# Kernel tuning notes

Measured on AMD Instinct MI355X. Metric: run time of the kernel, lower is better.

## Reference

```python
import jax, jax.numpy as jnp
import numpy as np

EPS = 1e-6
INF = 1e30  # stands in for 'no value' in the sparse C_bar lists of the torch code


def setup_inputs() -> dict:
    key = jax.random.key(0)
    M, N, D = 512, 256, 64
    kx, ky, kq = jax.random.split(key, 3)
    x = jax.random.normal(kx, (M, D), dtype=jnp.float32)
    y = jax.random.normal(ky, (N, D), dtype=jnp.float32)
    u = jax.random.uniform(kq, (N + 1, N), dtype=jnp.float32, minval=0.05, maxval=1.0)
    q = u / jnp.sum(u, axis=0, keepdims=True)  # column-stochastic jump probabilities
    return {"x": x, "y": y, "q": q}


def _pal_forward(x, y, q):
    M, N = x.shape[0], y.shape[0]
    dt = x.dtype

    # ---- compute_dists: pairwise L2 (p=2 norm), M x N ----
    diff = x[:, None, :] - y[None, :, :]
    dists = jnp.sqrt(jnp.sum(diff * diff, axis=2))

    # ---- compute_reachability: sequential accumulation over columns of q ----
    def reach_step(p, nb):
        return p + p[nb] * q[:, nb], None
    p0 = jnp.zeros(N + 1, dtype=dt).at[0].set(1.0)
    p, _ = jax.lax.scan(reach_step, p0, jnp.arange(N))
    p_back = p[:N][None, :] * q / (p[:, None] + EPS)  # (N+1, N)

    # ---- edge structure: ancestors n_bar < n with p_back > 0 (detached mask) ----
    tri = jnp.tril(jnp.ones((N, N), dtype=bool), k=-1)
    E = tri & (jax.lax.stop_gradient(p_back[:N]) > 0)   # (N, N): E[n, n_bar]
    w = jnp.where(E, p_back[:N], 0.0)                   # mixing weights

    ns = jnp.arange(1, N)

    def row_dp(d_row, base0, C_prev, Cbar_prev):
        """One row m of the lattice. C_prev: C[m-1] (N,), Cbar_prev: C_bar[m-1] (N,N).
        Returns C[m] (N,) and C_bar[m] (N,N) with INF at non-edge slots."""
        C0 = jnp.zeros(N, dtype=dt).at[0].set(d_row[0] + base0)

        def n_step(Ccur, n):
            # min over: C[m][n_bar] (insert y), C[m-1][n_bar] (match), C_bar[m-1][n][n_bar] (insert x)
            c_min = jnp.minimum(Ccur, jnp.minimum(C_prev, Cbar_prev[n]))  # (N,) over n_bar
            cbar = d_row[n] + c_min
            val = jnp.sum(jnp.where(E[n], w[n] * cbar, 0.0))
            return Ccur.at[n].set(val), jnp.where(E[n], cbar, INF)

        C_row, Cbar_rows = jax.lax.scan(n_step, C0, ns)
        Cbar = jnp.concatenate([jnp.full((1, N), INF, dt), Cbar_rows], axis=0)
        return C_row, Cbar

    # m = 0: no previous row -> previous-row candidates disabled via INF, C[0][0] = d[0,0]
    C_row0, Cbar0 = row_dp(dists[0], jnp.zeros((), dt), jnp.full(N, INF, dt), jnp.full((N, N), INF, dt))

    def m_step(carry, d_row):
        C_prev, Cbar_prev = carry
        C_row, Cbar = row_dp(d_row, C_prev[0], C_prev, Cbar_prev)  # C[m][0] = d[m,0] + C[m-1][0]
        return (C_row, Cbar), None

    (C_last, _), _ = jax.lax.scan(m_step, (C_row0, Cbar0), dists[1:])

    # expected cost of reaching END from each terminal n
    return jnp.sum(p_back[N] * C_last)


def reference(x, y, q):
    return _pal_forward(x, y, q)
```

## Files before the change

kernel.cpp:

```cpp
#include <hip/hip_runtime.h>

typedef float f4 __attribute__((ext_vector_type(4)));

#define Nn 256
#define Mm 512
#define Dd 64
#define EPSF 1e-6f
#define INFF 1e30f
#define BC 8
#define NCHUNK (Nn / BC)
#define R 16
#define NBLK 8
#define WVS 4
#define SST (NBLK * WVS)
#define SLOTS 4

#define OFF_D     0
#define OFF_QC    131072
#define OFF_P     (OFF_QC + 65792)
#define OFF_WT    (OFF_P + 260)
#define OFF_WS    (OFF_WT + 65536)
#define OFF_CBAR  (OFF_WS + 256)
#define OFF_CROW  (OFF_CBAR + 65536)
#define OFF_FLAG  (OFF_CROW + SST*Nn)

__device__ __forceinline__ int llc_load_int(const int* p) {
  int v;
  asm volatile("global_load_dword %0, %1, off sc0 sc1\n\ts_waitcnt vmcnt(0)"
               : "=v"(v) : "v"(p) : "memory");
  return v;
}
__device__ __forceinline__ void llc_store_int(int* p, int v) {
  asm volatile("global_store_dword %0, %1, off sc0 sc1" :: "v"(p), "v"(v) : "memory");
}
__device__ __forceinline__ void llc_load_cbar10(const float* b0, const float* cp,
                                                f4 c[8], f4& pl, f4& ph) {
  const float* b1 = b0 + 4 * Nn;
  asm volatile(
    "global_load_dwordx4 %0, %10, off sc0 sc1\n\t"
    "global_load_dwordx4 %1, %10, off offset:1024 sc0 sc1\n\t"
    "global_load_dwordx4 %2, %10, off offset:2048 sc0 sc1\n\t"
    "global_load_dwordx4 %3, %10, off offset:3072 sc0 sc1\n\t"
    "global_load_dwordx4 %4, %11, off sc0 sc1\n\t"
    "global_load_dwordx4 %5, %11, off offset:1024 sc0 sc1\n\t"
    "global_load_dwordx4 %6, %11, off offset:2048 sc0 sc1\n\t"
    "global_load_dwordx4 %7, %11, off offset:3072 sc0 sc1\n\t"
    "global_load_dwordx4 %8, %12, off sc0 sc1\n\t"
    "global_load_dwordx4 %9, %12, off offset:16 sc0 sc1\n\t"
    "s_waitcnt vmcnt(0)"
    : "=v"(c[0]), "=v"(c[1]), "=v"(c[2]), "=v"(c[3]),
      "=v"(c[4]), "=v"(c[5]), "=v"(c[6]), "=v"(c[7]),
      "=v"(pl), "=v"(ph)
    : "v"(b0), "v"(b1), "v"(cp)
    : "memory");
}
__device__ __forceinline__ void llc_store_cbar8(float* b0, const f4 c[8]) {
  float* b1 = b0 + 4 * Nn;
  asm volatile(
    "global_store_dwordx4 %8, %0, off sc0 sc1\n\t"
    "global_store_dwordx4 %8, %1, off offset:1024 sc0 sc1\n\t"
    "global_store_dwordx4 %8, %2, off offset:2048 sc0 sc1\n\t"
    "global_store_dwordx4 %8, %3, off offset:3072 sc0 sc1\n\t"
    "global_store_dwordx4 %9, %4, off sc0 sc1\n\t"
    "global_store_dwordx4 %9, %5, off offset:1024 sc0 sc1\n\t"
    "global_store_dwordx4 %9, %6, off offset:2048 sc0 sc1\n\t"
    "global_store_dwordx4 %9, %7, off offset:3072 sc0 sc1\n\t"
    "s_waitcnt vmcnt(0)"
    :: "v"(c[0]), "v"(c[1]), "v"(c[2]), "v"(c[3]),
       "v"(c[4]), "v"(c[5]), "v"(c[6]), "v"(c[7]),
       "v"(b0), "v"(b1)
    : "memory");
}
__device__ __forceinline__ float rdlane(float v, int l) {
  return __int_as_float(__builtin_amdgcn_readlane(__float_as_int(v), l));
}

__global__ __launch_bounds__(256) void k_pre(const float* __restrict__ x,
                                             const float* __restrict__ y,
                                             const float* __restrict__ q,
                                             float* __restrict__ ws) {
  const int b = blockIdx.x, t = threadIdx.x;
  if (b < Mm) {
    __shared__ float xs[Dd];
    if (t < Dd) xs[t] = x[b * Dd + t];
    __syncthreads();
    const float4* y4 = (const float4*)(y + t * Dd);
    float acc = 0.f;
#pragma unroll
    for (int k = 0; k < Dd / 4; k++) {
      float4 v = y4[k];
      float a0 = xs[4*k+0] - v.x, a1 = xs[4*k+1] - v.y;
      float a2 = xs[4*k+2] - v.z, a3 = xs[4*k+3] - v.w;
      acc += a0*a0 + a1*a1 + a2*a2 + a3*a3;
    }
    ws[OFF_D + b * Nn + t] = sqrtf(acc);
  } else if (b < Mm + 257) {
    const int j = b - Mm;
    ws[OFF_QC + t * 257 + j] = q[j * Nn + t];
  } else {
    ((int*)(ws + OFF_FLAG))[t] = 0;
  }
}

__global__ __launch_bounds__(256) void k_reach(const float* __restrict__ q, float* __restrict__ p_out) {
  __shared__ float p[257];
  __shared__ float vsnap[64];
  __shared__ float qtile[64][65];
  int tid = threadIdx.x;
  p[tid] = (tid == 0) ? 1.f : 0.f;
  if (tid == 0) p[256] = 0.f;
  __syncthreads();
  for (int g = 0; g < 4; g++) {
    int g0 = g * 64;
    for (int z = 0; z < 16; z++) {
      int idx = tid + z * 256, l = idx >> 6, k = idx & 63;
      qtile[k][l] = q[(g0 + l) * Nn + g0 + k];
    }
    __syncthreads();
    if (tid < 64) {
      float pv = p[g0 + tid];
      for (int k = 0; k < 64; k++) {
        float v = __shfl(pv, k, 64);
        if (tid == k) vsnap[k] = v;
        pv += v * qtile[k][tid];
      }
    }
    __syncthreads();
    float4 qs[16];
    const float4* qrow = (const float4*)(q + tid * Nn + g0);
#pragma unroll
    for (int i = 0; i < 16; i++) qs[i] = qrow[i];
    float acc = p[tid];
#pragma unroll
    for (int i = 0; i < 16; i++) {
      acc += vsnap[4*i+0] * qs[i].x;
      acc += vsnap[4*i+1] * qs[i].y;
      acc += vsnap[4*i+2] * qs[i].z;
      acc += vsnap[4*i+3] * qs[i].w;
    }
    float acc2 = 0.f;
    if (tid == 0) {
      acc2 = p[256];
      const float4* qlast = (const float4*)(q + 256 * Nn + g0);
#pragma unroll
      for (int i = 0; i < 16; i++) {
        float4 v = qlast[i];
        acc2 += vsnap[4*i+0] * v.x + vsnap[4*i+1] * v.y
              + vsnap[4*i+2] * v.z + vsnap[4*i+3] * v.w;
      }
    }
    __syncthreads();
    p[tid] = acc;
    if (tid == 0) p[256] = acc2;
    __syncthreads();
  }
  p_out[tid] = p[tid];
  if (tid == 0) p_out[256] = p[256];
}

__global__ __launch_bounds__(256) void k_wbuild(const float* __restrict__ qc, const float* __restrict__ p,
                                                float* __restrict__ wT) {
  int t = blockIdx.x, n = threadIdx.x;
  float v = 0.f;
  if (t < n) v = p[t] * qc[t * 257 + n] / (p[n] + EPSF);
  wT[t * Nn + n] = v;
}

__global__ __launch_bounds__(256, 1) void k_main(const float* __restrict__ d,
                                                 const float* __restrict__ wT,
                                                 float* __restrict__ cbarG,
                                                 float* __restrict__ crowG,
                                                 int* __restrict__ flags,
                                                 const float* __restrict__ q,
                                                 const float* __restrict__ p,
                                                 float* __restrict__ out) {
  __shared__ __align__(16) float sbuf[SLOTS][BC * Nn];
  __shared__ __align__(16) float crow_lds[WVS][SLOTS][BC];
  __shared__ __align__(16) float crow_fin[Nn];

  const int tid  = threadIdx.x;
  const int wave = tid >> 6;
  const int lane = tid & 63;
  const int blk  = blockIdx.x;
  const int stage = blk * WVS + wave;
  const int m0 = stage * R;

  f4 dl[R], S[R];
#pragma unroll
  for (int r = 0; r < R; r++) {
    dl[r] = *(const f4*)(d + (m0 + r) * Nn + 4 * lane);
    S[r] = (f4){0.f, 0.f, 0.f, 0.f};
  }
  f4 Wt = (f4){0.f, 0.f, 0.f, 0.f};
#pragma unroll 8
  for (int t = 0; t < Nn; t++)
    Wt += *(const f4*)(wT + t * Nn + 4 * lane);

#pragma clang loop unroll(disable)
  for (int s = 0; s < NCHUNK + WVS - 1; s++) {
    const int j = s - wave;
    if (j >= 0 && j < NCHUNK) {
      f4 wv[BC];
#pragma unroll
      for (int tt = 0; tt < BC; tt++)
        wv[tt] = *(const f4*)(wT + (j * BC + tt) * Nn + 4 * lane);

      f4 c[BC], cpl, cph;
      float* lsl = &sbuf[j & (SLOTS - 1)][0] + 4 * lane;

      if (wave == 0) {
        if (blk > 0) {
          const int* fp = flags + (blk - 1) * NCHUNK + j;
          while (llc_load_int(fp) == 0) __builtin_amdgcn_s_sleep(1);
          llc_load_cbar10(cbarG + (size_t)j * BC * Nn + 4 * lane,
                          crowG + (blk - 1) * Nn + j * BC, c, cpl, cph);
        } else {
          cpl = (f4){INFF, INFF, INFF, INFF};
          cph = cpl;
#pragma unroll
          for (int tt = 0; tt < BC; tt++) c[tt] = cpl;
        }
      } else {
#pragma unroll
        for (int tt = 0; tt < BC; tt++) c[tt] = *(const f4*)(lsl + tt * Nn);
        const float* cr = &crow_lds[wave - 1][j & (SLOTS - 1)][0];
        cpl = *(const f4*)cr;
        cph = *(const f4*)(cr + 4);
      }

      f4 clast4;
      const bool isJ0 = (j == 0);
#pragma unroll
      for (int tt = 0; tt < BC; tt++) {
        const int owner = 2 * j + (tt >> 2);
        const int comp = tt & 3;
        const bool isT0 = isJ0 && (tt == 0);

        float up = (tt < 4) ? cpl[comp] : cph[comp];
        float prcMin = up;
        float prcVal = up;
        if (isT0 && stage == 0) prcVal = 0.f;
        float cml[R];
#pragma unroll
        for (int r = 0; r < R; r++) {
          float Cv;
          if (isT0) Cv = dl[r][0] + prcVal;
          else      Cv = fmaf(dl[r][comp], Wt[comp], S[r][comp]);
          cml[r] = fminf(Cv, prcMin);
          prcVal = Cv;
          prcMin = Cv;
        }
        float cmB[R];
#pragma unroll
        for (int r = 0; r < R; r++) cmB[r] = rdlane(cml[r], owner);
        float clastv = rdlane(prcVal, owner);
        if (lane == owner) clast4[comp] = clastv;

#pragma unroll
        for (int k = 0; k < 4; k++) {
          float w_ = wv[tt][k];
          if (w_ > 0.f) {
            float cbv = c[tt][k];
#pragma unroll
            for (int r = 0; r < R; r++) {
              float a = fminf(cmB[r], cbv);
              S[r][k] = fmaf(w_, a, S[r][k]);
              cbv = dl[r][k] + a;
            }
            c[tt][k] = cbv;
          }
        }
      }

      if (wave < WVS - 1) {
#pragma unroll
        for (int tt = 0; tt < BC; tt++) *(f4*)(lsl + tt * Nn) = c[tt];
        if (lane == 2 * j || lane == 2 * j + 1)
          *(f4*)&crow_lds[wave][j & (SLOTS - 1)][(lane & 1) * 4] = clast4;
      } else if (blk < NBLK - 1) {
        if (lane == 2 * j || lane == 2 * j + 1) {
          float* cp = crowG + blk * Nn + j * BC + (lane & 1) * 4;
          asm volatile("global_store_dwordx4 %0, %1, off sc0 sc1" :: "v"(cp), "v"(clast4) : "memory");
        }
        llc_store_cbar8(cbarG + (size_t)j * BC * Nn + 4 * lane, c);
        if (lane == 0) llc_store_int(flags + blk * NCHUNK + j, 1);
      } else {
        if (lane == 2 * j || lane == 2 * j + 1)
          *(f4*)&crow_fin[j * BC + (lane & 1) * 4] = clast4;
      }
    }
    __syncthreads();
  }

  if (blk == NBLK - 1) {
    float fw = p[tid] * q[Nn * Nn + tid] / (p[Nn] + EPSF);
    crow_fin[tid] *= fw;
    __syncthreads();
    for (int sft = 128; sft > 0; sft >>= 1) {
      if (tid < sft) crow_fin[tid] += crow_fin[tid + sft];
      __syncthreads();
    }
    if (tid == 0) out[0] = crow_fin[0];
  }
}

extern "C" void kernel_launch(void* const* d_in, const int* in_sizes, int n_in,
                              void* d_out, int out_size, void* d_ws, size_t ws_size,
                              hipStream_t stream) {
  const float* x = (const float*)d_in[0];
  const float* y = (const float*)d_in[1];
  const float* q = (const float*)d_in[2];
  float* ws = (float*)d_ws;
  float* out = (float*)d_out;
  hipLaunchKernelGGL(k_pre,   dim3(Mm + 257 + 1), dim3(256), 0, stream, x, y, q, ws);
  hipLaunchKernelGGL(k_reach, dim3(1),   dim3(256), 0, stream, q, ws + OFF_P);
  hipLaunchKernelGGL(k_wbuild,dim3(Nn),  dim3(256), 0, stream, ws + OFF_QC, ws + OFF_P,
                     ws + OFF_WT);
  hipLaunchKernelGGL(k_main,  dim3(NBLK), dim3(256), 0, stream, ws + OFF_D, ws + OFF_WT,
                     ws + OFF_CBAR, ws + OFF_CROW, (int*)(ws + OFF_FLAG),
                     q, ws + OFF_P, out);
}
```

Baseline: 466.7 us.

## Fuse reachability and weight-building kernels into the main wavefront kernel

Removes the separate single-block reachability kernel and the weight-matrix build kernel. Each main-kernel block now recomputes the reachability vector redundantly in shared memory and derives mixing weights on the fly from the transposed q and p, instead of reading a precomputed wT. The transposed q stride is padded to 260 so rows are 16-byte aligned for vector loads. This saves two launches and a global round trip, at the cost of every block repeating the serial reachability scan and doing extra arithmetic per chunk.

```diff
diff --git a/kernel.cpp b/kernel.cpp
--- a/kernel.cpp
+++ b/kernel.cpp
@@ -14,13 +14,11 @@
 #define WVS 4
 #define SST (NBLK * WVS)
 #define SLOTS 4
+#define QSTR 260
 
 #define OFF_D     0
 #define OFF_QC    131072
-#define OFF_P     (OFF_QC + 65792)
-#define OFF_WT    (OFF_P + 260)
-#define OFF_WS    (OFF_WT + 65536)
-#define OFF_CBAR  (OFF_WS + 256)
+#define OFF_CBAR  (OFF_QC + 67072)
 #define OFF_CROW  (OFF_CBAR + 65536)
 #define OFF_FLAG  (OFF_CROW + SST*Nn)
 
@@ -96,19 +94,35 @@
     ws[OFF_D + b * Nn + t] = sqrtf(acc);
   } else if (b < Mm + 257) {
     const int j = b - Mm;
-    ws[OFF_QC + t * 257 + j] = q[j * Nn + t];
+    ws[OFF_QC + t * QSTR + j] = q[j * Nn + t];
   } else {
     ((int*)(ws + OFF_FLAG))[t] = 0;
   }
 }
 
-__global__ __launch_bounds__(256) void k_reach(const float* __restrict__ q, float* __restrict__ p_out) {
-  __shared__ float p[257];
+__global__ __launch_bounds__(256, 1) void k_main(const float* __restrict__ d,
+                                                 const float* __restrict__ qc,
+                                                 float* __restrict__ cbarG,
+                                                 float* __restrict__ crowG,
+                                                 int* __restrict__ flags,
+                                                 const float* __restrict__ q,
+                                                 float* __restrict__ out) {
+  __shared__ __align__(16) float sbuf[SLOTS][BC * Nn];
+  __shared__ __align__(16) float crow_lds[WVS][SLOTS][BC];
+  __shared__ __align__(16) float crow_fin[Nn];
+  __shared__ float pl[257];
   __shared__ float vsnap[64];
   __shared__ float qtile[64][65];
-  int tid = threadIdx.x;
-  p[tid] = (tid == 0) ? 1.f : 0.f;
-  if (tid == 0) p[256] = 0.f;
+
+  const int tid  = threadIdx.x;
+  const int wave = tid >> 6;
+  const int lane = tid & 63;
+  const int blk  = blockIdx.x;
+  const int stage = blk * WVS + wave;
+  const int m0 = stage * R;
+
+  pl[tid] = (tid == 0) ? 1.f : 0.f;
+  if (tid == 0) pl[256] = 0.f;
   __syncthreads();
   for (int g = 0; g < 4; g++) {
     int g0 = g * 64;
@@ -118,7 +132,7 @@
     }
     __syncthreads();
     if (tid < 64) {
-      float pv = p[g0 + tid];
+      float pv = pl[g0 + tid];
       for (int k = 0; k < 64; k++) {
         float v = __shfl(pv, k, 64);
         if (tid == k) vsnap[k] = v;
@@ -130,7 +144,7 @@
     const float4* qrow = (const float4*)(q + tid * Nn + g0);
 #pragma unroll
     for (int i = 0; i < 16; i++) qs[i] = qrow[i];
-    float acc = p[tid];
+    float acc = pl[tid];
 #pragma unroll
     for (int i = 0; i < 16; i++) {
       acc += vsnap[4*i+0] * qs[i].x;
@@ -140,7 +154,7 @@
     }
     float acc2 = 0.f;
     if (tid == 0) {
-      acc2 = p[256];
+      acc2 = pl[256];
       const float4* qlast = (const float4*)(q + 256 * Nn + g0);
 #pragma unroll
       for (int i = 0; i < 16; i++) {
@@ -150,40 +164,25 @@
       }
     }
     __syncthreads();
-    p[tid] = acc;
-    if (tid == 0) p[256] = acc2;
-    __syncthreads();
-  }
-  p_out[tid] = p[tid];
-  if (tid == 0) p_out[256] = p[256];
-}
-
-__global__ __launch_bounds__(256) void k_wbuild(const float* __restrict__ qc, const float* __restrict__ p,
-                                                float* __restrict__ wT) {
-  int t = blockIdx.x, n = threadIdx.x;
-  float v = 0.f;
-  if (t < n) v = p[t] * qc[t * 257 + n] / (p[n] + EPSF);
-  wT[t * Nn + n] = v;
-}
-
-__global__ __launch_bounds__(256, 1) void k_main(const float* __restrict__ d,
-                                                 const float* __restrict__ wT,
-                                                 float* __restrict__ cbarG,
-                                                 float* __restrict__ crowG,
-                                                 int* __restrict__ flags,
-                                                 const float* __restrict__ q,
-                                                 const float* __restrict__ p,
-                                                 float* __restrict__ out) {
-  __shared__ __align__(16) float sbuf[SLOTS][BC * Nn];
-  __shared__ __align__(16) float crow_lds[WVS][SLOTS][BC];
-  __shared__ __align__(16) float crow_fin[Nn];
-
-  const int tid  = threadIdx.x;
-  const int wave = tid >> 6;
-  const int lane = tid & 63;
-  const int blk  = blockIdx.x;
-  const int stage = blk * WVS + wave;
-  const int m0 = stage * R;
+    pl[tid] = acc;
+    if (tid == 0) pl[256] = acc2;
+    __syncthreads();
+  }
+
+  const int col0 = 4 * lane;
+  f4 rp;
+#pragma unroll
+  for (int k = 0; k < 4; k++) rp[k] = 1.f / (pl[col0 + k] + EPSF);
+  f4 Wt = (f4){0.f, 0.f, 0.f, 0.f};
+#pragma unroll 4
+  for (int t = 0; t < Nn; t++) {
+    float pt = pl[t];
+    f4 qv = *(const f4*)(qc + t * QSTR + col0);
+#pragma unroll
+    for (int k = 0; k < 4; k++)
+      if (t < col0 + k) Wt[k] += pt * qv[k];
+  }
+  Wt *= rp;
 
   f4 dl[R], S[R];
 #pragma unroll
@@ -191,10 +190,6 @@
     dl[r] = *(const f4*)(d + (m0 + r) * Nn + 4 * lane);
     S[r] = (f4){0.f, 0.f, 0.f, 0.f};
   }
-  f4 Wt = (f4){0.f, 0.f, 0.f, 0.f};
-#pragma unroll 8
-  for (int t = 0; t < Nn; t++)
-    Wt += *(const f4*)(wT + t * Nn + 4 * lane);
 
 #pragma clang loop unroll(disable)
   for (int s = 0; s < NCHUNK + WVS - 1; s++) {
@@ -202,8 +197,16 @@
     if (j >= 0 && j < NCHUNK) {
       f4 wv[BC];
 #pragma unroll
-      for (int tt = 0; tt < BC; tt++)
-        wv[tt] = *(const f4*)(wT + (j * BC + tt) * Nn + 4 * lane);
+      for (int tt = 0; tt < BC; tt++) {
+        const int t = j * BC + tt;
+        const float pt = pl[t];
+        f4 qv = *(const f4*)(qc + t * QSTR + col0);
+        f4 w;
+#pragma unroll
+        for (int k = 0; k < 4; k++)
+          w[k] = (t < col0 + k) ? pt * qv[k] * rp[k] : 0.f;
+        wv[tt] = w;
+      }
 
       f4 c[BC], cpl, cph;
       float* lsl = &sbuf[j & (SLOTS - 1)][0] + 4 * lane;
@@ -293,7 +296,7 @@
   }
 
   if (blk == NBLK - 1) {
-    float fw = p[tid] * q[Nn * Nn + tid] / (p[Nn] + EPSF);
+    float fw = pl[tid] * q[Nn * Nn + tid] / (pl[256] + EPSF);
     crow_fin[tid] *= fw;
     __syncthreads();
     for (int sft = 128; sft > 0; sft >>= 1) {
@@ -313,10 +316,6 @@
   float* ws = (float*)d_ws;
   float* out = (float*)d_out;
   hipLaunchKernelGGL(k_pre,   dim3(Mm + 257 + 1), dim3(256), 0, stream, x, y, q, ws);
-  hipLaunchKernelGGL(k_reach, dim3(1),   dim3(256), 0, stream, q, ws + OFF_P);
-  hipLaunchKernelGGL(k_wbuild,dim3(Nn),  dim3(256), 0, stream, ws + OFF_QC, ws + OFF_P,
-                     ws + OFF_WT);
-  hipLaunchKernelGGL(k_main,  dim3(NBLK), dim3(256), 0, stream, ws + OFF_D, ws + OFF_WT,
-                     ws + OFF_CBAR, ws + OFF_CROW, (int*)(ws + OFF_FLAG),
-                     q, ws + OFF_P, out);
-}
+  hipLaunchKernelGGL(k_main,  dim3(NBLK), dim3(256), 0, stream, ws + OFF_D, ws + OFF_QC,
+                     ws + OFF_CBAR, ws + OFF_CROW, (int*)(ws + OFF_FLAG), q, out);
+}
```

New measurement: 470.7 us. About the same (+0.9%).
